# Kernel optimization log

Hardware: AMD Instinct MI355X
Metric: run time of the kernel (lower is better)

## Reference

```python
import jax, jax.numpy as jnp
import numpy as np

D_MODEL = 768
NUM_HEADS = 12
D_HEAD = D_MODEL // NUM_HEADS


def setup_inputs() -> dict:
    key = jax.random.key(0)
    ks = jax.random.split(key, 11)
    B, S = 1, 4096
    s = 1.0 / np.sqrt(D_MODEL)
    inp = {
        'q': jax.random.normal(ks[0], (B, S, D_MODEL), dtype=jnp.float32),
        'k': jax.random.normal(ks[1], (B, S, D_MODEL), dtype=jnp.float32),
        'v': jax.random.normal(ks[2], (B, S, D_MODEL), dtype=jnp.float32),
        'wq': jax.random.normal(ks[3], (D_MODEL, D_MODEL), dtype=jnp.float32) * s,
        'bq': jnp.zeros((D_MODEL,), dtype=jnp.float32),
        'wk': jax.random.normal(ks[4], (D_MODEL, D_MODEL), dtype=jnp.float32) * s,
        'bk': jnp.zeros((D_MODEL,), dtype=jnp.float32),
        'wv': jax.random.normal(ks[5], (D_MODEL, D_MODEL), dtype=jnp.float32) * s,
        'bv': jnp.zeros((D_MODEL,), dtype=jnp.float32),
        'wo': jax.random.normal(ks[6], (D_MODEL, D_MODEL), dtype=jnp.float32) * s,
        'bo': jnp.zeros((D_MODEL,), dtype=jnp.float32),
    }
    return inp


def reference(q, k, v, wq, bq, wk, bk, wv, bv, wo, bo):
    B, S, _ = q.shape
    # linear projections (torch Linear: x @ W^T + b)
    qh = (q @ wq.T + bq).reshape(B, S, NUM_HEADS, D_HEAD).transpose(0, 2, 1, 3)
    kh = (k @ wk.T + bk).reshape(B, S, NUM_HEADS, D_HEAD).transpose(0, 2, 1, 3)
    vh = (v @ wv.T + bv).reshape(B, S, NUM_HEADS, D_HEAD).transpose(0, 2, 1, 3)
    scores = jnp.einsum('bhqd,bhkd->bhqk', qh, kh) / jnp.sqrt(jnp.float32(D_HEAD))
    causal = jnp.tril(jnp.ones((S, S), dtype=bool))  # [S,S] causal mask
    scores = jnp.where(causal, scores, jnp.finfo(scores.dtype).min)
    attn = jax.nn.softmax(scores, axis=-1)  # dropout omitted (eval mode)
    out = jnp.einsum('bhqk,bhkd->bhqd', attn, vh)
    out = out.transpose(0, 2, 1, 3).reshape(B, S, D_MODEL)
    return out @ wo.T + bo
```

## Files before the change

### kernel.cpp

```cpp
#include <hip/hip_runtime.h>
#include <stdint.h>

typedef __attribute__((ext_vector_type(8))) short short8;
typedef __attribute__((ext_vector_type(4))) float float4v;
typedef __attribute__((ext_vector_type(2))) uint32_t uint32x2;
typedef __attribute__((ext_vector_type(4))) uint32_t uint32x4;

__device__ __forceinline__ unsigned short f2bf(float f) {
  union { float f; uint32_t u; } v;
  v.f = f;
  uint32_t u = v.u;
  return (unsigned short)((u + 0x7fffu + ((u >> 16) & 1u)) >> 16);
}

__device__ __forceinline__ uint32_t pkbf(float a, float b) {
#if __has_builtin(__builtin_amdgcn_cvt_pk_bf16_f32)
  typedef __attribute__((ext_vector_type(2))) __bf16 bf16x2;
  bf16x2 r = __builtin_amdgcn_cvt_pk_bf16_f32(a, b);
  union { bf16x2 v; uint32_t u; } c;
  c.v = r;
  return c.u;
#else
  return (uint32_t)f2bf(a) | ((uint32_t)f2bf(b) << 16);
#endif
}

__device__ __forceinline__ float fexp2(float x) {
#if __has_builtin(__builtin_amdgcn_exp2f)
  return __builtin_amdgcn_exp2f(x);
#else
  return exp2f(x);
#endif
}

__device__ __forceinline__ void gll16(const unsigned short* g, unsigned short* l) {
  __builtin_amdgcn_global_load_lds(
      (const __attribute__((address_space(1))) void*)g,
      (__attribute__((address_space(3))) void*)l, 16, 0, 0);
}

__global__ __launch_bounds__(256) void cvt_bf16x(
    const float* __restrict__ s0, unsigned short* __restrict__ o0,
    const float* __restrict__ s1, unsigned short* __restrict__ o1,
    const float* __restrict__ s2, unsigned short* __restrict__ o2,
    const float* __restrict__ s3, unsigned short* __restrict__ o3,
    int n8) {
  const int y = blockIdx.y;
  const float* in = y == 0 ? s0 : y == 1 ? s1 : y == 2 ? s2 : s3;
  unsigned short* out = y == 0 ? o0 : y == 1 ? o1 : y == 2 ? o2 : o3;
  int i = blockIdx.x * 256 + threadIdx.x;
  if (i >= n8) return;
  const float4v* p = (const float4v*)(in + (size_t)i * 8);
  float4v a = p[0], b = p[1];
  uint32x4 o;
  o[0] = pkbf(a[0], a[1]);
  o[1] = pkbf(a[2], a[3]);
  o[2] = pkbf(b[0], b[1]);
  o[3] = pkbf(b[2], b[3]);
  *(uint32x4*)(out + (size_t)i * 8) = o;
}

__global__ __launch_bounds__(256) void gemm_qkv(
    const unsigned short* __restrict__ xq, const unsigned short* __restrict__ xk,
    const unsigned short* __restrict__ xv,
    const unsigned short* __restrict__ wqb, const unsigned short* __restrict__ wkb,
    const unsigned short* __restrict__ wvb,
    const float* __restrict__ bq, const float* __restrict__ bk,
    const float* __restrict__ bv,
    unsigned short* __restrict__ Qp, unsigned short* __restrict__ Kp,
    unsigned short* __restrict__ Vt, float qscale)
{
  __shared__ unsigned short As[128 * 64];
  __shared__ unsigned short Ws[128 * 64];
  const int z = blockIdx.z;
  const unsigned short* A = z == 0 ? xq : z == 1 ? xk : xv;
  const unsigned short* W = z == 0 ? wqb : z == 1 ? wkb : wvb;
  const float* bias = z == 0 ? bq : z == 1 ? bk : bv;
  const float osc = z == 0 ? qscale : 1.0f;
  const int M = 4096, N = 768, K = 768;
  const int tid = threadIdx.x, wave = tid >> 6, lane = tid & 63;
  const int g = lane >> 4, l16 = lane & 15;
  const int m0 = blockIdx.x * 128, n0 = blockIdx.y * 128;
  const int wm = (wave >> 1) * 64, wn = (wave & 1) * 64;
  const int srow0 = wave * 32 + (lane >> 3);
  const int skg = lane & 7;
  const int sw = l16 & 7;

  float4v acc[4][4] = {};

  for (int k0 = 0; k0 < K; k0 += 64) {
    if (k0) __syncthreads();
    #pragma unroll
    for (int c = 0; c < 4; ++c) {
      const int row = srow0 + c * 8;
      const int kg = skg ^ (row & 7);
      gll16(A + (size_t)(m0 + row) * K + k0 + kg * 8, &As[(wave * 32 + c * 8) * 64]);
      gll16(W + (size_t)(n0 + row) * K + k0 + kg * 8, &Ws[(wave * 32 + c * 8) * 64]);
    }
    __syncthreads();
    #pragma unroll
    for (int kk = 0; kk < 2; ++kk) {
      const int kg = ((kk * 4 + g) ^ sw) * 8;
      short8 a[4], b[4];
      #pragma unroll
      for (int i = 0; i < 4; ++i) a[i] = *(const short8*)&As[(wm + i * 16 + l16) * 64 + kg];
      #pragma unroll
      for (int j = 0; j < 4; ++j) b[j] = *(const short8*)&Ws[(wn + j * 16 + l16) * 64 + kg];
      #pragma unroll
      for (int i = 0; i < 4; ++i)
        #pragma unroll
        for (int j = 0; j < 4; ++j)
          acc[i][j] = __builtin_amdgcn_mfma_f32_16x16x32_bf16(a[i], b[j], acc[i][j], 0, 0, 0);
    }
  }

  if (z < 2) {
    unsigned short* O = z == 0 ? Qp : Kp;
    #pragma unroll
    for (int j = 0; j < 4; ++j) {
      const int n = n0 + wn + j * 16 + l16;
      const float bb = bias[n];
      #pragma unroll
      for (int i = 0; i < 4; ++i) {
        const int mb = m0 + wm + i * 16 + g * 4;
        #pragma unroll
        for (int r = 0; r < 4; ++r)
          O[(size_t)(mb + r) * N + n] = f2bf((acc[i][j][r] + bb) * osc);
      }
    }
  } else {
    #pragma unroll
    for (int j = 0; j < 4; ++j) {
      const int n = n0 + wn + j * 16 + l16;
      const float bb = bias[n];
      #pragma unroll
      for (int i = 0; i < 4; ++i) {
        const int mb = m0 + wm + i * 16 + g * 4;
        uint32x2 pk;
        pk[0] = pkbf(acc[i][j][0] + bb, acc[i][j][1] + bb);
        pk[1] = pkbf(acc[i][j][2] + bb, acc[i][j][3] + bb);
        *(uint32x2*)(Vt + (size_t)n * M + mb) = pk;
      }
    }
  }
}

__global__ __launch_bounds__(256) void gemm_out(
    const unsigned short* __restrict__ A, const unsigned short* __restrict__ W,
    const float* __restrict__ bias, float* __restrict__ Out)
{
  __shared__ unsigned short As[128 * 64];
  __shared__ unsigned short Ws[128 * 64];
  const int M = 4096, N = 768, K = 768;
  const int tid = threadIdx.x, wave = tid >> 6, lane = tid & 63;
  const int g = lane >> 4, l16 = lane & 15;
  const int m0 = blockIdx.x * 128, n0 = blockIdx.y * 128;
  const int wm = (wave >> 1) * 64, wn = (wave & 1) * 64;
  const int srow0 = wave * 32 + (lane >> 3);
  const int skg = lane & 7;
  const int sw = l16 & 7;

  float4v acc[4][4] = {};

  for (int k0 = 0; k0 < K; k0 += 64) {
    if (k0) __syncthreads();
    #pragma unroll
    for (int c = 0; c < 4; ++c) {
      const int row = srow0 + c * 8;
      const int kg = skg ^ (row & 7);
      gll16(A + (size_t)(m0 + row) * K + k0 + kg * 8, &As[(wave * 32 + c * 8) * 64]);
      gll16(W + (size_t)(n0 + row) * K + k0 + kg * 8, &Ws[(wave * 32 + c * 8) * 64]);
    }
    __syncthreads();
    #pragma unroll
    for (int kk = 0; kk < 2; ++kk) {
      const int kg = ((kk * 4 + g) ^ sw) * 8;
      short8 a[4], b[4];
      #pragma unroll
      for (int i = 0; i < 4; ++i) a[i] = *(const short8*)&As[(wm + i * 16 + l16) * 64 + kg];
      #pragma unroll
      for (int j = 0; j < 4; ++j) b[j] = *(const short8*)&Ws[(wn + j * 16 + l16) * 64 + kg];
      #pragma unroll
      for (int i = 0; i < 4; ++i)
        #pragma unroll
        for (int j = 0; j < 4; ++j)
          acc[i][j] = __builtin_amdgcn_mfma_f32_16x16x32_bf16(a[i], b[j], acc[i][j], 0, 0, 0);
    }
  }

  #pragma unroll
  for (int j = 0; j < 4; ++j) {
    const int n = n0 + wn + j * 16 + l16;
    const float bb = bias[n];
    #pragma unroll
    for (int i = 0; i < 4; ++i) {
      const int mb = m0 + wm + i * 16 + g * 4;
      #pragma unroll
      for (int r = 0; r < 4; ++r)
        Out[(size_t)(mb + r) * N + n] = acc[i][j][r] + bb;
    }
  }
}

__global__ __launch_bounds__(256, 4) void flash_attn(
    const unsigned short* __restrict__ Qp,
    const unsigned short* __restrict__ Kp,
    const unsigned short* __restrict__ Vt,
    unsigned short* __restrict__ AO)
{
  __shared__ unsigned short lds_k[2][64 * 64];
  __shared__ unsigned short lds_v[2][64 * 64];
  __shared__ unsigned short lds_p[4][16 * 64];
  const int S = 4096, DM = 768;

  const int x = blockIdx.x & 7, s = blockIdx.x >> 3;
  const int w = 96 * x + s;
  const int h = w >> 6;
  const int v = w & 63;
  const int u = v & 31;
  const int zz = (u & 1) ? (31 - (u >> 1)) : (u >> 1);
  const int qtile = (v & 32) ? (63 - zz) : zz;

  const int tid = threadIdx.x, wave = tid >> 6, lane = tid & 63;
  const int g = lane >> 4, l16 = lane & 15;
  const int qlocal = wave * 16 + l16;
  const int qrow = qtile * 64 + qlocal;
  const int sw = l16 & 7;

  short8 qf0 = *(const short8*)(Qp + (size_t)qrow * DM + h * 64 + 0  + g * 8);
  short8 qf1 = *(const short8*)(Qp + (size_t)qrow * DM + h * 64 + 32 + g * 8);

  float4v o[4] = {};
  float lsum = 0.0f;

  const int strow = wave * 16 + (lane >> 3);
  const int skg = lane & 7;

  #pragma unroll
  for (int c = 0; c < 2; ++c) {
    const int row = strow + c * 8;
    const int kg = skg ^ (row & 7);
    gll16(Kp + (size_t)row * DM + h * 64 + kg * 8, &lds_k[0][(wave * 16 + c * 8) * 64]);
    gll16(Vt + (size_t)(h * 64 + row) * S + kg * 8, &lds_v[0][(wave * 16 + c * 8) * 64]);
  }
  __syncthreads();

  for (int kb = 0; kb <= qtile; ++kb) {
    const int cur = kb & 1;
    if (kb < qtile) {
      const int nb = cur ^ 1;
      #pragma unroll
      for (int c = 0; c < 2; ++c) {
        const int row = strow + c * 8;
        const int kg = skg ^ (row & 7);
        gll16(Kp + (size_t)((kb + 1) * 64 + row) * DM + h * 64 + kg * 8,
              &lds_k[nb][(wave * 16 + c * 8) * 64]);
        gll16(Vt + (size_t)(h * 64 + row) * S + (kb + 1) * 64 + kg * 8,
              &lds_v[nb][(wave * 16 + c * 8) * 64]);
      }
    }
    const unsigned short* kc = lds_k[cur];
    const unsigned short* vc = lds_v[cur];

    float4v sf[4];
    #pragma unroll
    for (int mt = 0; mt < 4; ++mt) {
      float4v a = {};
      short8 ka0 = *(const short8*)&kc[(mt * 16 + l16) * 64 + ((0 + g) ^ sw) * 8];
      a = __builtin_amdgcn_mfma_f32_16x16x32_bf16(ka0, qf0, a, 0, 0, 0);
      short8 ka1 = *(const short8*)&kc[(mt * 16 + l16) * 64 + ((4 + g) ^ sw) * 8];
      a = __builtin_amdgcn_mfma_f32_16x16x32_bf16(ka1, qf1, a, 0, 0, 0);
      sf[mt] = a;
    }

    if (kb == qtile) {
      #pragma unroll
      for (int mt = 0; mt < 4; ++mt)
        #pragma unroll
        for (int r = 0; r < 4; ++r) {
          const int klocal = mt * 16 + g * 4 + r;
          sf[mt][r] = (klocal <= qlocal) ? sf[mt][r] : -1e30f;
        }
    }

    #pragma unroll
    for (int mt = 0; mt < 4; ++mt)
      #pragma unroll
      for (int r = 0; r < 4; ++r) {
        const float p = fexp2(sf[mt][r]);
        sf[mt][r] = p;
        lsum += p;
      }

    unsigned short* pw = lds_p[wave];
    #pragma unroll
    for (int mt = 0; mt < 4; ++mt) {
      uint32x2 pp;
      pp[0] = pkbf(sf[mt][0], sf[mt][1]);
      pp[1] = pkbf(sf[mt][2], sf[mt][3]);
      const int kgp = mt * 2 + (g >> 1);
      *(uint32x2*)&pw[l16 * 64 + ((kgp ^ sw) * 8) + (g & 1) * 4] = pp;
    }
    __builtin_amdgcn_wave_barrier();

    #pragma unroll
    for (int ks2 = 0; ks2 < 2; ++ks2) {
      short8 pf = *(const short8*)&pw[l16 * 64 + (((ks2 * 4 + g) ^ sw) * 8)];
      #pragma unroll
      for (int dt = 0; dt < 4; ++dt) {
        short8 va = *(const short8*)&vc[(dt * 16 + l16) * 64 + (((ks2 * 4 + g) ^ sw) * 8)];
        o[dt] = __builtin_amdgcn_mfma_f32_16x16x32_bf16(va, pf, o[dt], 0, 0, 0);
      }
    }

    __syncthreads();
  }

  lsum += __shfl_xor(lsum, 16);
  lsum += __shfl_xor(lsum, 32);
  const float inv = 1.0f / lsum;
  #pragma unroll
  for (int dt = 0; dt < 4; ++dt) {
    uint32x2 ov;
    ov[0] = pkbf(o[dt][0] * inv, o[dt][1] * inv);
    ov[1] = pkbf(o[dt][2] * inv, o[dt][3] * inv);
    *(uint32x2*)(AO + (size_t)qrow * DM + h * 64 + dt * 16 + g * 4) = ov;
  }
}

extern "C" void kernel_launch(void* const* d_in, const int* in_sizes, int n_in,
                              void* d_out, int out_size, void* d_ws, size_t ws_size,
                              hipStream_t stream) {
  const float* q  = (const float*)d_in[0];
  const float* k  = (const float*)d_in[1];
  const float* v  = (const float*)d_in[2];
  const float* wq = (const float*)d_in[3];
  const float* bq = (const float*)d_in[4];
  const float* wk = (const float*)d_in[5];
  const float* bk = (const float*)d_in[6];
  const float* wv = (const float*)d_in[7];
  const float* bv = (const float*)d_in[8];
  const float* wo = (const float*)d_in[9];
  const float* bo = (const float*)d_in[10];
  float* out = (float*)d_out;

  const int S = 4096, D = 768;
  unsigned short* Qp  = (unsigned short*)d_ws;
  unsigned short* Kp  = Qp  + (size_t)S * D;
  unsigned short* Vt  = Kp  + (size_t)S * D;
  unsigned short* AO  = Vt  + (size_t)S * D;
  unsigned short* xq  = AO  + (size_t)S * D;
  unsigned short* xk  = xq  + (size_t)S * D;
  unsigned short* xv  = xk  + (size_t)S * D;
  unsigned short* wqb = xv  + (size_t)S * D;
  unsigned short* wkb = wqb + (size_t)D * D;
  unsigned short* wvb = wkb + (size_t)D * D;
  unsigned short* wob = wvb + (size_t)D * D;

  const int nx8 = S * D / 8;
  const int nw8 = D * D / 8;
  dim3 blk(256);
  cvt_bf16x<<<dim3(nx8 / 256, 3), blk, 0, stream>>>(q, xq, k, xk, v, xv, v, xv, nx8);
  cvt_bf16x<<<dim3(nw8 / 256, 4), blk, 0, stream>>>(wq, wqb, wk, wkb, wv, wvb, wo, wob, nw8);

  const float SC = 0.125f * 1.44269504089f;
  gemm_qkv<<<dim3(32, 6, 3), blk, 0, stream>>>(xq, xk, xv, wqb, wkb, wvb,
                                               bq, bk, bv, Qp, Kp, Vt, SC);
  flash_attn<<<dim3(768), blk, 0, stream>>>(Qp, Kp, Vt, AO);
  gemm_out<<<dim3(32, 6), blk, 0, stream>>>(AO, wob, bo, out);
}
```

Measured before the change: 221.7 us.

## Fuse fp32-to-bf16 conversion into GEMMs and process two query chunks per wave

```diff
diff --git a/kernel.cpp b/kernel.cpp
--- a/kernel.cpp
+++ b/kernel.cpp
@@ -39,32 +39,11 @@
       (__attribute__((address_space(3))) void*)l, 16, 0, 0);
 }
 
-__global__ __launch_bounds__(256) void cvt_bf16x(
-    const float* __restrict__ s0, unsigned short* __restrict__ o0,
-    const float* __restrict__ s1, unsigned short* __restrict__ o1,
-    const float* __restrict__ s2, unsigned short* __restrict__ o2,
-    const float* __restrict__ s3, unsigned short* __restrict__ o3,
-    int n8) {
-  const int y = blockIdx.y;
-  const float* in = y == 0 ? s0 : y == 1 ? s1 : y == 2 ? s2 : s3;
-  unsigned short* out = y == 0 ? o0 : y == 1 ? o1 : y == 2 ? o2 : o3;
-  int i = blockIdx.x * 256 + threadIdx.x;
-  if (i >= n8) return;
-  const float4v* p = (const float4v*)(in + (size_t)i * 8);
-  float4v a = p[0], b = p[1];
-  uint32x4 o;
-  o[0] = pkbf(a[0], a[1]);
-  o[1] = pkbf(a[2], a[3]);
-  o[2] = pkbf(b[0], b[1]);
-  o[3] = pkbf(b[2], b[3]);
-  *(uint32x4*)(out + (size_t)i * 8) = o;
-}
-
 __global__ __launch_bounds__(256) void gemm_qkv(
-    const unsigned short* __restrict__ xq, const unsigned short* __restrict__ xk,
-    const unsigned short* __restrict__ xv,
-    const unsigned short* __restrict__ wqb, const unsigned short* __restrict__ wkb,
-    const unsigned short* __restrict__ wvb,
+    const float* __restrict__ xq, const float* __restrict__ xk,
+    const float* __restrict__ xv,
+    const float* __restrict__ wq, const float* __restrict__ wk,
+    const float* __restrict__ wv,
     const float* __restrict__ bq, const float* __restrict__ bk,
     const float* __restrict__ bv,
     unsigned short* __restrict__ Qp, unsigned short* __restrict__ Kp,
@@ -73,69 +52,97 @@
   __shared__ unsigned short As[128 * 64];
   __shared__ unsigned short Ws[128 * 64];
   const int z = blockIdx.z;
-  const unsigned short* A = z == 0 ? xq : z == 1 ? xk : xv;
-  const unsigned short* W = z == 0 ? wqb : z == 1 ? wkb : wvb;
+  const float* A32 = z == 0 ? xq : z == 1 ? xk : xv;
+  const float* W32 = z == 0 ? wq : z == 1 ? wk : wv;
   const float* bias = z == 0 ? bq : z == 1 ? bk : bv;
-  const float osc = z == 0 ? qscale : 1.0f;
   const int M = 4096, N = 768, K = 768;
   const int tid = threadIdx.x, wave = tid >> 6, lane = tid & 63;
   const int g = lane >> 4, l16 = lane & 15;
+  const int sw = l16 & 7;
   const int m0 = blockIdx.x * 128, n0 = blockIdx.y * 128;
-  const int wm = (wave >> 1) * 64, wn = (wave & 1) * 64;
-  const int srow0 = wave * 32 + (lane >> 3);
-  const int skg = lane & 7;
-  const int sw = l16 & 7;
+  const int wn_q = (wave >> 1) * 64, wm_q = (wave & 1) * 64;
+  const int srow = tid >> 1, kof = (tid & 1) * 32;
+  const int rs = srow & 7;
 
   float4v acc[4][4] = {};
 
   for (int k0 = 0; k0 < K; k0 += 64) {
     if (k0) __syncthreads();
-    #pragma unroll
-    for (int c = 0; c < 4; ++c) {
-      const int row = srow0 + c * 8;
-      const int kg = skg ^ (row & 7);
-      gll16(A + (size_t)(m0 + row) * K + k0 + kg * 8, &As[(wave * 32 + c * 8) * 64]);
-      gll16(W + (size_t)(n0 + row) * K + k0 + kg * 8, &Ws[(wave * 32 + c * 8) * 64]);
+    float4v av[8], wv8[8];
+    {
+      const float* pa = A32 + (size_t)(m0 + srow) * K + k0 + kof;
+      const float* pw = W32 + (size_t)(n0 + srow) * K + k0 + kof;
+      #pragma unroll
+      for (int i = 0; i < 8; ++i) {
+        av[i]  = *(const float4v*)(pa + i * 4);
+        wv8[i] = *(const float4v*)(pw + i * 4);
+      }
+    }
+    #pragma unroll
+    for (int gi = 0; gi < 4; ++gi) {
+      const int slot = (((tid & 1) * 4 + gi) ^ rs) * 8;
+      uint32x4 pa, pw;
+      pa[0] = pkbf(av[gi*2][0], av[gi*2][1]);
+      pa[1] = pkbf(av[gi*2][2], av[gi*2][3]);
+      pa[2] = pkbf(av[gi*2+1][0], av[gi*2+1][1]);
+      pa[3] = pkbf(av[gi*2+1][2], av[gi*2+1][3]);
+      pw[0] = pkbf(wv8[gi*2][0], wv8[gi*2][1]);
+      pw[1] = pkbf(wv8[gi*2][2], wv8[gi*2][3]);
+      pw[2] = pkbf(wv8[gi*2+1][0], wv8[gi*2+1][1]);
+      pw[3] = pkbf(wv8[gi*2+1][2], wv8[gi*2+1][3]);
+      *(uint32x4*)&As[srow * 64 + slot] = pa;
+      *(uint32x4*)&Ws[srow * 64 + slot] = pw;
     }
     __syncthreads();
     #pragma unroll
     for (int kk = 0; kk < 2; ++kk) {
       const int kg = ((kk * 4 + g) ^ sw) * 8;
-      short8 a[4], b[4];
-      #pragma unroll
-      for (int i = 0; i < 4; ++i) a[i] = *(const short8*)&As[(wm + i * 16 + l16) * 64 + kg];
-      #pragma unroll
-      for (int j = 0; j < 4; ++j) b[j] = *(const short8*)&Ws[(wn + j * 16 + l16) * 64 + kg];
-      #pragma unroll
-      for (int i = 0; i < 4; ++i)
-        #pragma unroll
-        for (int j = 0; j < 4; ++j)
-          acc[i][j] = __builtin_amdgcn_mfma_f32_16x16x32_bf16(a[i], b[j], acc[i][j], 0, 0, 0);
+      short8 xf[4], wf[4];
+      #pragma unroll
+      for (int t = 0; t < 4; ++t) {
+        xf[t] = *(const short8*)&As[(wm_q + t * 16 + l16) * 64 + kg];
+        wf[t] = *(const short8*)&Ws[(wn_q + t * 16 + l16) * 64 + kg];
+      }
+      if (z < 2) {
+        #pragma unroll
+        for (int i = 0; i < 4; ++i)
+          #pragma unroll
+          for (int j = 0; j < 4; ++j)
+            acc[i][j] = __builtin_amdgcn_mfma_f32_16x16x32_bf16(wf[i], xf[j], acc[i][j], 0, 0, 0);
+      } else {
+        #pragma unroll
+        for (int i = 0; i < 4; ++i)
+          #pragma unroll
+          for (int j = 0; j < 4; ++j)
+            acc[i][j] = __builtin_amdgcn_mfma_f32_16x16x32_bf16(xf[i], wf[j], acc[i][j], 0, 0, 0);
+      }
     }
   }
 
   if (z < 2) {
     unsigned short* O = z == 0 ? Qp : Kp;
+    const float osc = z == 0 ? qscale : 1.0f;
+    #pragma unroll
+    for (int i = 0; i < 4; ++i) {
+      const int nb = n0 + wn_q + i * 16 + 4 * g;
+      const float4v bb = *(const float4v*)&bias[nb];
+      #pragma unroll
+      for (int j = 0; j < 4; ++j) {
+        const int m = m0 + wm_q + j * 16 + l16;
+        uint32x2 pk;
+        pk[0] = pkbf((acc[i][j][0] + bb[0]) * osc, (acc[i][j][1] + bb[1]) * osc);
+        pk[1] = pkbf((acc[i][j][2] + bb[2]) * osc, (acc[i][j][3] + bb[3]) * osc);
+        *(uint32x2*)(O + (size_t)m * N + nb) = pk;
+      }
+    }
+  } else {
     #pragma unroll
     for (int j = 0; j < 4; ++j) {
-      const int n = n0 + wn + j * 16 + l16;
+      const int n = n0 + wn_q + j * 16 + l16;
       const float bb = bias[n];
       #pragma unroll
       for (int i = 0; i < 4; ++i) {
-        const int mb = m0 + wm + i * 16 + g * 4;
-        #pragma unroll
-        for (int r = 0; r < 4; ++r)
-          O[(size_t)(mb + r) * N + n] = f2bf((acc[i][j][r] + bb) * osc);
-      }
-    }
-  } else {
-    #pragma unroll
-    for (int j = 0; j < 4; ++j) {
-      const int n = n0 + wn + j * 16 + l16;
-      const float bb = bias[n];
-      #pragma unroll
-      for (int i = 0; i < 4; ++i) {
-        const int mb = m0 + wm + i * 16 + g * 4;
+        const int mb = m0 + wm_q + i * 16 + 4 * g;
         uint32x2 pk;
         pk[0] = pkbf(acc[i][j][0] + bb, acc[i][j][1] + bb);
         pk[1] = pkbf(acc[i][j][2] + bb, acc[i][j][3] + bb);
@@ -145,64 +152,7 @@
   }
 }
 
-__global__ __launch_bounds__(256) void gemm_out(
-    const unsigned short* __restrict__ A, const unsigned short* __restrict__ W,
-    const float* __restrict__ bias, float* __restrict__ Out)
-{
-  __shared__ unsigned short As[128 * 64];
-  __shared__ unsigned short Ws[128 * 64];
-  const int M = 4096, N = 768, K = 768;
-  const int tid = threadIdx.x, wave = tid >> 6, lane = tid & 63;
-  const int g = lane >> 4, l16 = lane & 15;
-  const int m0 = blockIdx.x * 128, n0 = blockIdx.y * 128;
-  const int wm = (wave >> 1) * 64, wn = (wave & 1) * 64;
-  const int srow0 = wave * 32 + (lane >> 3);
-  const int skg = lane & 7;
-  const int sw = l16 & 7;
-
-  float4v acc[4][4] = {};
-
-  for (int k0 = 0; k0 < K; k0 += 64) {
-    if (k0) __syncthreads();
-    #pragma unroll
-    for (int c = 0; c < 4; ++c) {
-      const int row = srow0 + c * 8;
-      const int kg = skg ^ (row & 7);
-      gll16(A + (size_t)(m0 + row) * K + k0 + kg * 8, &As[(wave * 32 + c * 8) * 64]);
-      gll16(W + (size_t)(n0 + row) * K + k0 + kg * 8, &Ws[(wave * 32 + c * 8) * 64]);
-    }
-    __syncthreads();
-    #pragma unroll
-    for (int kk = 0; kk < 2; ++kk) {
-      const int kg = ((kk * 4 + g) ^ sw) * 8;
-      short8 a[4], b[4];
-      #pragma unroll
-      for (int i = 0; i < 4; ++i) a[i] = *(const short8*)&As[(wm + i * 16 + l16) * 64 + kg];
-      #pragma unroll
-      for (int j = 0; j < 4; ++j) b[j] = *(const short8*)&Ws[(wn + j * 16 + l16) * 64 + kg];
-      #pragma unroll
-      for (int i = 0; i < 4; ++i)
-        #pragma unroll
-        for (int j = 0; j < 4; ++j)
-          acc[i][j] = __builtin_amdgcn_mfma_f32_16x16x32_bf16(a[i], b[j], acc[i][j], 0, 0, 0);
-    }
-  }
-
-  #pragma unroll
-  for (int j = 0; j < 4; ++j) {
-    const int n = n0 + wn + j * 16 + l16;
-    const float bb = bias[n];
-    #pragma unroll
-    for (int i = 0; i < 4; ++i) {
-      const int mb = m0 + wm + i * 16 + g * 4;
-      #pragma unroll
-      for (int r = 0; r < 4; ++r)
-        Out[(size_t)(mb + r) * N + n] = acc[i][j][r] + bb;
-    }
-  }
-}
-
-__global__ __launch_bounds__(256, 4) void flash_attn(
+__global__ __launch_bounds__(256, 2) void flash_attn(
     const unsigned short* __restrict__ Qp,
     const unsigned short* __restrict__ Kp,
     const unsigned short* __restrict__ Vt,
@@ -210,28 +160,31 @@
 {
   __shared__ unsigned short lds_k[2][64 * 64];
   __shared__ unsigned short lds_v[2][64 * 64];
-  __shared__ unsigned short lds_p[4][16 * 64];
+  __shared__ unsigned short lds_p[4][32 * 64];
   const int S = 4096, DM = 768;
 
-  const int x = blockIdx.x & 7, s = blockIdx.x >> 3;
-  const int w = 96 * x + s;
-  const int h = w >> 6;
-  const int v = w & 63;
-  const int u = v & 31;
-  const int zz = (u & 1) ? (31 - (u >> 1)) : (u >> 1);
-  const int qtile = (v & 32) ? (63 - zz) : zz;
+  const int gid = blockIdx.x;
+  const int x = gid & 7, r = gid >> 3;
+  const bool heavy = r < 24;
+  const int p = x * 24 + (heavy ? r : r - 24);
+  const int h = p >> 4, tp = p & 15;
+  const int qtile = heavy ? 31 - tp : tp;
 
   const int tid = threadIdx.x, wave = tid >> 6, lane = tid & 63;
   const int g = lane >> 4, l16 = lane & 15;
-  const int qlocal = wave * 16 + l16;
-  const int qrow = qtile * 64 + qlocal;
   const int sw = l16 & 7;
-
-  short8 qf0 = *(const short8*)(Qp + (size_t)qrow * DM + h * 64 + 0  + g * 8);
-  short8 qf1 = *(const short8*)(Qp + (size_t)qrow * DM + h * 64 + 32 + g * 8);
-
-  float4v o[4] = {};
-  float lsum = 0.0f;
+  const int qbase = qtile * 128 + wave * 32;
+
+  short8 qf[2][2];
+  #pragma unroll
+  for (int qc = 0; qc < 2; ++qc) {
+    const unsigned short* qp = Qp + (size_t)(qbase + qc * 16 + l16) * DM + h * 64;
+    qf[qc][0] = *(const short8*)(qp + g * 8);
+    qf[qc][1] = *(const short8*)(qp + 32 + g * 8);
+  }
+
+  float4v o[2][4] = {};
+  float lsum[2] = {0.0f, 0.0f};
 
   const int strow = wave * 16 + (lane >> 3);
   const int skg = lane & 7;
@@ -245,9 +198,10 @@
   }
   __syncthreads();
 
-  for (int kb = 0; kb <= qtile; ++kb) {
+  const int kmax = 2 * qtile + 1;
+  for (int kb = 0; kb <= kmax; ++kb) {
     const int cur = kb & 1;
-    if (kb < qtile) {
+    if (kb < kmax) {
       const int nb = cur ^ 1;
       #pragma unroll
       for (int c = 0; c < 2; ++c) {
@@ -262,69 +216,167 @@
     const unsigned short* kc = lds_k[cur];
     const unsigned short* vc = lds_v[cur];
 
-    float4v sf[4];
+    float4v sf[2][4];
     #pragma unroll
     for (int mt = 0; mt < 4; ++mt) {
-      float4v a = {};
       short8 ka0 = *(const short8*)&kc[(mt * 16 + l16) * 64 + ((0 + g) ^ sw) * 8];
-      a = __builtin_amdgcn_mfma_f32_16x16x32_bf16(ka0, qf0, a, 0, 0, 0);
       short8 ka1 = *(const short8*)&kc[(mt * 16 + l16) * 64 + ((4 + g) ^ sw) * 8];
-      a = __builtin_amdgcn_mfma_f32_16x16x32_bf16(ka1, qf1, a, 0, 0, 0);
-      sf[mt] = a;
-    }
-
-    if (kb == qtile) {
+      #pragma unroll
+      for (int qc = 0; qc < 2; ++qc) {
+        float4v a = {};
+        a = __builtin_amdgcn_mfma_f32_16x16x32_bf16(ka0, qf[qc][0], a, 0, 0, 0);
+        a = __builtin_amdgcn_mfma_f32_16x16x32_bf16(ka1, qf[qc][1], a, 0, 0, 0);
+        sf[qc][mt] = a;
+      }
+    }
+
+    if ((kb + 1) * 64 > qbase) {
+      #pragma unroll
+      for (int qc = 0; qc < 2; ++qc) {
+        const int q = qbase + qc * 16 + l16;
+        #pragma unroll
+        for (int mt = 0; mt < 4; ++mt)
+          #pragma unroll
+          for (int rr = 0; rr < 4; ++rr) {
+            const int key = kb * 64 + mt * 16 + 4 * g + rr;
+            sf[qc][mt][rr] = (key <= q) ? sf[qc][mt][rr] : -1e30f;
+          }
+      }
+    }
+
+    #pragma unroll
+    for (int qc = 0; qc < 2; ++qc)
       #pragma unroll
       for (int mt = 0; mt < 4; ++mt)
         #pragma unroll
-        for (int r = 0; r < 4; ++r) {
-          const int klocal = mt * 16 + g * 4 + r;
-          sf[mt][r] = (klocal <= qlocal) ? sf[mt][r] : -1e30f;
+        for (int rr = 0; rr < 4; ++rr) {
+          const float pe = fexp2(sf[qc][mt][rr]);
+          sf[qc][mt][rr] = pe;
+          lsum[qc] += pe;
         }
-    }
-
-    #pragma unroll
-    for (int mt = 0; mt < 4; ++mt)
-      #pragma unroll
-      for (int r = 0; r < 4; ++r) {
-        const float p = fexp2(sf[mt][r]);
-        sf[mt][r] = p;
-        lsum += p;
-      }
 
     unsigned short* pw = lds_p[wave];
     #pragma unroll
-    for (int mt = 0; mt < 4; ++mt) {
-      uint32x2 pp;
-      pp[0] = pkbf(sf[mt][0], sf[mt][1]);
-      pp[1] = pkbf(sf[mt][2], sf[mt][3]);
-      const int kgp = mt * 2 + (g >> 1);
-      *(uint32x2*)&pw[l16 * 64 + ((kgp ^ sw) * 8) + (g & 1) * 4] = pp;
+    for (int qc = 0; qc < 2; ++qc) {
+      #pragma unroll
+      for (int mt = 0; mt < 4; ++mt) {
+        uint32x2 pp;
+        pp[0] = pkbf(sf[qc][mt][0], sf[qc][mt][1]);
+        pp[1] = pkbf(sf[qc][mt][2], sf[qc][mt][3]);
+        const int kgp = mt * 2 + (g >> 1);
+        *(uint32x2*)&pw[(qc * 16 + l16) * 64 + ((kgp ^ sw) * 8) + (g & 1) * 4] = pp;
+      }
     }
     __builtin_amdgcn_wave_barrier();
 
     #pragma unroll
     for (int ks2 = 0; ks2 < 2; ++ks2) {
-      short8 pf = *(const short8*)&pw[l16 * 64 + (((ks2 * 4 + g) ^ sw) * 8)];
+      short8 pf[2];
+      #pragma unroll
+      for (int qc = 0; qc < 2; ++qc)
+        pf[qc] = *(const short8*)&pw[(qc * 16 + l16) * 64 + (((ks2 * 4 + g) ^ sw) * 8)];
       #pragma unroll
       for (int dt = 0; dt < 4; ++dt) {
         short8 va = *(const short8*)&vc[(dt * 16 + l16) * 64 + (((ks2 * 4 + g) ^ sw) * 8)];
-        o[dt] = __builtin_amdgcn_mfma_f32_16x16x32_bf16(va, pf, o[dt], 0, 0, 0);
+        #pragma unroll
+        for (int qc = 0; qc < 2; ++qc)
+          o[qc][dt] = __builtin_amdgcn_mfma_f32_16x16x32_bf16(va, pf[qc], o[qc][dt], 0, 0, 0);
       }
     }
 
     __syncthreads();
   }
 
-  lsum += __shfl_xor(lsum, 16);
-  lsum += __shfl_xor(lsum, 32);
-  const float inv = 1.0f / lsum;
   #pragma unroll
-  for (int dt = 0; dt < 4; ++dt) {
-    uint32x2 ov;
-    ov[0] = pkbf(o[dt][0] * inv, o[dt][1] * inv);
-    ov[1] = pkbf(o[dt][2] * inv, o[dt][3] * inv);
-    *(uint32x2*)(AO + (size_t)qrow * DM + h * 64 + dt * 16 + g * 4) = ov;
+  for (int qc = 0; qc < 2; ++qc) {
+    float L = lsum[qc];
+    L += __shfl_xor(L, 16);
+    L += __shfl_xor(L, 32);
+    const float inv = 1.0f / L;
+    const int q = qbase + qc * 16 + l16;
+    #pragma unroll
+    for (int dt = 0; dt < 4; ++dt) {
+      uint32x2 ov;
+      ov[0] = pkbf(o[qc][dt][0] * inv, o[qc][dt][1] * inv);
+      ov[1] = pkbf(o[qc][dt][2] * inv, o[qc][dt][3] * inv);
+      *(uint32x2*)(AO + (size_t)q * DM + h * 64 + dt * 16 + 4 * g) = ov;
+    }
+  }
+}
+
+__global__ __launch_bounds__(256) void gemm_out(
+    const unsigned short* __restrict__ A, const float* __restrict__ W32,
+    const float* __restrict__ bias, float* __restrict__ Out)
+{
+  __shared__ unsigned short As[128 * 64];
+  __shared__ unsigned short Ws[64 * 64];
+  const int N = 768, K = 768;
+  const int tid = threadIdx.x, wave = tid >> 6, lane = tid & 63;
+  const int g = lane >> 4, l16 = lane & 15;
+  const int sw = l16 & 7;
+  const int m0 = blockIdx.x * 128, n0 = blockIdx.y * 64;
+  const int strow = wave * 32 + (lane >> 3);
+  const int skg = lane & 7;
+  const int wrow = tid >> 2, wkof = (tid & 3) * 16;
+  const int wrs = wrow & 7;
+
+  float4v acc[4][2] = {};
+
+  for (int k0 = 0; k0 < K; k0 += 64) {
+    if (k0) __syncthreads();
+    #pragma unroll
+    for (int c = 0; c < 4; ++c) {
+      const int row = strow + c * 8;
+      const int kg = skg ^ (row & 7);
+      gll16(A + (size_t)(m0 + row) * K + k0 + kg * 8, &As[(wave * 32 + c * 8) * 64]);
+    }
+    {
+      const float* pw = W32 + (size_t)(n0 + wrow) * K + k0 + wkof;
+      float4v w0 = *(const float4v*)pw, w1 = *(const float4v*)(pw + 4);
+      float4v w2 = *(const float4v*)(pw + 8), w3 = *(const float4v*)(pw + 12);
+      #pragma unroll
+      for (int gi = 0; gi < 2; ++gi) {
+        const int slot = (((tid & 3) * 2 + gi) ^ wrs) * 8;
+        uint32x4 pk;
+        const float4v& lo = gi ? w2 : w0;
+        const float4v& hi = gi ? w3 : w1;
+        pk[0] = pkbf(lo[0], lo[1]);
+        pk[1] = pkbf(lo[2], lo[3]);
+        pk[2] = pkbf(hi[0], hi[1]);
+        pk[3] = pkbf(hi[2], hi[3]);
+        *(uint32x4*)&Ws[wrow * 64 + slot] = pk;
+      }
+    }
+    __syncthreads();
+    #pragma unroll
+    for (int kk = 0; kk < 2; ++kk) {
+      const int kg = ((kk * 4 + g) ^ sw) * 8;
+      short8 wf[4], xf[2];
+      #pragma unroll
+      for (int i = 0; i < 4; ++i) wf[i] = *(const short8*)&Ws[(i * 16 + l16) * 64 + kg];
+      #pragma unroll
+      for (int j = 0; j < 2; ++j)
+        xf[j] = *(const short8*)&As[(wave * 32 + j * 16 + l16) * 64 + kg];
+      #pragma unroll
+      for (int i = 0; i < 4; ++i)
+        #pragma unroll
+        for (int j = 0; j < 2; ++j)
+          acc[i][j] = __builtin_amdgcn_mfma_f32_16x16x32_bf16(wf[i], xf[j], acc[i][j], 0, 0, 0);
+    }
+  }
+
+  #pragma unroll
+  for (int i = 0; i < 4; ++i) {
+    const int nb = n0 + i * 16 + 4 * g;
+    const float4v bb = *(const float4v*)&bias[nb];
+    #pragma unroll
+    for (int j = 0; j < 2; ++j) {
+      const int m = m0 + wave * 32 + j * 16 + l16;
+      float4v ov;
+      #pragma unroll
+      for (int rr = 0; rr < 4; ++rr) ov[rr] = acc[i][j][rr] + bb[rr];
+      *(float4v*)(Out + (size_t)m * N + nb) = ov;
+    }
   }
 }
 
@@ -345,27 +397,15 @@
   float* out = (float*)d_out;
 
   const int S = 4096, D = 768;
-  unsigned short* Qp  = (unsigned short*)d_ws;
-  unsigned short* Kp  = Qp  + (size_t)S * D;
-  unsigned short* Vt  = Kp  + (size_t)S * D;
-  unsigned short* AO  = Vt  + (size_t)S * D;
-  unsigned short* xq  = AO  + (size_t)S * D;
-  unsigned short* xk  = xq  + (size_t)S * D;
-  unsigned short* xv  = xk  + (size_t)S * D;
-  unsigned short* wqb = xv  + (size_t)S * D;
-  unsigned short* wkb = wqb + (size_t)D * D;
-  unsigned short* wvb = wkb + (size_t)D * D;
-  unsigned short* wob = wvb + (size_t)D * D;
-
-  const int nx8 = S * D / 8;
-  const int nw8 = D * D / 8;
+  unsigned short* Qp = (unsigned short*)d_ws;
+  unsigned short* Kp = Qp + (size_t)S * D;
+  unsigned short* Vt = Kp + (size_t)S * D;
+  unsigned short* AO = Vt + (size_t)S * D;
+
+  const float SC = 0.125f * 1.44269504089f;
   dim3 blk(256);
-  cvt_bf16x<<<dim3(nx8 / 256, 3), blk, 0, stream>>>(q, xq, k, xk, v, xv, v, xv, nx8);
-  cvt_bf16x<<<dim3(nw8 / 256, 4), blk, 0, stream>>>(wq, wqb, wk, wkb, wv, wvb, wo, wob, nw8);
-
-  const float SC = 0.125f * 1.44269504089f;
-  gemm_qkv<<<dim3(32, 6, 3), blk, 0, stream>>>(xq, xk, xv, wqb, wkb, wvb,
-                                               bq, bk, bv, Qp, Kp, Vt, SC);
-  flash_attn<<<dim3(768), blk, 0, stream>>>(Qp, Kp, Vt, AO);
-  gemm_out<<<dim3(32, 6), blk, 0, stream>>>(AO, wob, bo, out);
-}
+  gemm_qkv<<<dim3(32, 6, 3), blk, 0, stream>>>(q, k, v, wq, wk, wv, bq, bk, bv,
+                                               Qp, Kp, Vt, SC);
+  flash_attn<<<dim3(384), blk, 0, stream>>>(Qp, Kp, Vt, AO);
+  gemm_out<<<dim3(32, 12), blk, 0, stream>>>(AO, wo, bo, out);
+}
```

Result: slower. 277.8 us (+25.3%).
